# Kernel tuning notes

Measured on AMD Instinct MI355X. Metric: run time of the kernel, lower is better.

Reference implementation:

```python
import jax, jax.numpy as jnp
import numpy as np

K = 9  # 3x3 kernel field

def _conv(x, w, b, pad):
    out = jax.lax.conv_general_dilated(x, w, (1, 1), ((pad, pad), (pad, pad)),
                                       dimension_numbers=('NCHW', 'OIHW', 'NCHW'))
    return out + b[None, :, None, None]

def _conv_transpose(x, w, b):
    # torch ConvTranspose2d(k=3, stride=2, padding=1, output_padding=1); w: [Cin, Cout, 3, 3]
    wk = jnp.flip(jnp.transpose(w, (1, 0, 2, 3)), axis=(2, 3))  # [Cout, Cin, 3, 3]
    out = jax.lax.conv_general_dilated(x, wk, (1, 1), ((1, 2), (1, 2)),
                                       lhs_dilation=(2, 2),
                                       dimension_numbers=('NCHW', 'OIHW', 'NCHW'))
    return out + b[None, :, None, None]

def _modulated_deform_conv(x, offset, mask, w, b):
    # x: [B,C,H,W], offset: [B,2K,H,W] (y,x interleaved per kernel point, row-major),
    # mask: [B,K,H,W], w: [O,C,3,3]; stride=1, pad=1, dilation=1
    B, C, H, W = x.shape
    O = w.shape[0]
    off = offset.reshape(B, K, 2, H, W)
    ky, kx = jnp.meshgrid(jnp.arange(3), jnp.arange(3), indexing='ij')
    base_y = (jnp.arange(H)[None, :, None] - 1 + ky.reshape(K, 1, 1)).astype(x.dtype)  # [K,H,1]
    base_x = (jnp.arange(W)[None, None, :] - 1 + kx.reshape(K, 1, 1)).astype(x.dtype)  # [K,1,W]
    py = off[:, :, 0] + base_y[None]  # [B,K,H,W]
    px = off[:, :, 1] + base_x[None]
    y0 = jnp.floor(py); x0 = jnp.floor(px)
    wy = py - y0; wx = px - x0
    y0i = y0.astype(jnp.int32); x0i = x0.astype(jnp.int32)
    flat = x.reshape(B, C, H * W)

    def gather(yi, xi):
        valid = ((yi >= 0) & (yi < H) & (xi >= 0) & (xi < W)).astype(x.dtype)
        idx = jnp.clip(yi, 0, H - 1) * W + jnp.clip(xi, 0, W - 1)  # [B,K,H,W]
        g = jax.vmap(lambda im, ix: im[:, ix])(flat, idx.reshape(B, -1))  # [B,C,K*H*W]
        return g.reshape(B, C, K, H, W) * valid[:, None]

    v = (gather(y0i, x0i)         * ((1 - wy) * (1 - wx))[:, None]
       + gather(y0i, x0i + 1)     * ((1 - wy) * wx)[:, None]
       + gather(y0i + 1, x0i)     * (wy * (1 - wx))[:, None]
       + gather(y0i + 1, x0i + 1) * (wy * wx)[:, None])
    v = v * mask[:, None]  # modulation
    out = jnp.einsum('bckhw,ock->bohw', v, w.reshape(O, C, K))
    return out + b[None, :, None, None]

def setup_inputs() -> dict:
    key = jax.random.key(0)
    ks = jax.random.split(key, 8)
    B, Cin, Cout, H, W = 4, 128, 64, 64, 64
    return {
        'high_feature': jax.random.normal(ks[0], (B, Cin, H, W), jnp.float32),
        'low_feature': jax.random.normal(ks[1], (B, Cout, 2 * H, 2 * W), jnp.float32),
        'w_up': jax.random.normal(ks[2], (Cin, Cout, 3, 3), jnp.float32) * 0.03,
        'b_up': jnp.zeros((Cout,), jnp.float32),
        'w_off': jax.random.normal(ks[3], (3 * K, 2 * Cout, 3, 3), jnp.float32) * 0.02,
        'b_off': jnp.zeros((3 * K,), jnp.float32),
        'w_align': jax.random.normal(ks[4], (Cout, Cout, 3, 3), jnp.float32) * 0.04,
        'b_align': jnp.zeros((Cout,), jnp.float32),
    }

def reference(high_feature, low_feature, w_up, b_up, w_off, b_off, w_align, b_align):
    up = _conv_transpose(high_feature, w_up, b_up)            # [B,Cout,2H,2W]
    fo = _conv(jnp.concatenate([up, low_feature], axis=1), w_off, b_off, 1)
    offset, mask = fo[:, :2 * K], fo[:, 2 * K:]
    mask = 2.0 * jax.nn.sigmoid(mask)
    aligned = _modulated_deform_conv(up, offset, mask, w_align, b_align)
    aligned = jnp.where(aligned >= 0, aligned, 0.2 * aligned)  # LeakyReLU(0.2)
    return jnp.concatenate([aligned, low_feature], axis=1)
```

## Files before the change

### kernel.cpp

```cpp
#include <hip/hip_runtime.h>
#include <math.h>

namespace {
constexpr int B   = 4;
constexpr int CIN = 128;
constexpr int CO  = 64;
constexpr int HF  = 64;
constexpr int HO  = 128;
constexpr int HW  = HO * HO;
constexpr int NOFF = 27;

constexpr size_t UPB  = 0;
constexpr size_t LOB  = UPB + (size_t)B * HW * CO / 2;
constexpr size_t HBF  = LOB + (size_t)B * HW * CO / 2;
constexpr size_t WFRG = HBF + (size_t)B * HF * HF * CIN / 2;
constexpr size_t WFUP = WFRG + (size_t)(4 * 18 * 64 * 8) / 2;
constexpr size_t WFOF = WFUP + (size_t)(9 * 4 * 4 * 64 * 8) / 2;
}

using half8 = __attribute__((ext_vector_type(8))) _Float16;
using h2    = __attribute__((ext_vector_type(2))) _Float16;
using f32x4 = __attribute__((ext_vector_type(4))) float;

__device__ __forceinline__ unsigned short f2h16(float f) {
  return __builtin_bit_cast(unsigned short, (_Float16)f);
}
__device__ __forceinline__ unsigned pkh(float a, float b) {
  return __builtin_bit_cast(unsigned, __builtin_amdgcn_cvt_pkrtz(a, b));
}
__device__ __forceinline__ h2 u2h(unsigned u) { return __builtin_bit_cast(h2, u); }
__device__ __forceinline__ unsigned h2u(h2 v) { return __builtin_bit_cast(unsigned, v); }
__device__ __forceinline__ h2 dup_lo(unsigned u) {
  return u2h(__builtin_amdgcn_perm(u, u, 0x01000100u));
}
__device__ __forceinline__ h2 dup_hi(unsigned u) {
  return u2h(__builtin_amdgcn_perm(u, u, 0x03020302u));
}

__global__ __launch_bounds__(256) void k_prep(const float* __restrict__ high,
                                              const float* __restrict__ wup,
                                              const float* __restrict__ woff,
                                              const float* __restrict__ wal,
                                              float* __restrict__ ws) {
  __shared__ unsigned short tl2[32][66];
  const int bid = blockIdx.x;
  const int t = threadIdx.x;

  if (bid < 288) {
    int i = bid * 256 + t;
    if (i < 4 * 18 * 64 * 8) {
      int j = i & 7; int t2 = i >> 3;
      int lane = t2 & 63; int t3 = t2 >> 6;
      int kb = t3 % 18; int w = t3 / 18;
      int tap = kb >> 1;
      int c = (kb & 1) * 32 + ((lane >> 4) << 3) + j;
      int o = (w << 4) + (lane & 15);
      unsigned short* wfrag = (unsigned short*)(ws + WFRG);
      wfrag[i] = f2h16(wal[((size_t)o * CO + c) * 9 + tap]);
    }
    if (i < 9 * 4 * 4 * 64 * 8) {
      int j = i & 7; int lane = (i >> 3) & 63; int w = (i >> 9) & 3;
      int ch = (i >> 11) & 3; int rr = i >> 13;
      int c = ch * 32 + ((lane >> 4) << 3) + j;
      int o = w * 16 + (lane & 15);
      unsigned short* wfup = (unsigned short*)(ws + WFUP);
      wfup[i] = f2h16(wup[((size_t)c * CO + o) * 9 + rr]);
    }
    if (i < 9 * 4 * 2 * 64 * 8) {
      int j = i & 7; int lane = (i >> 3) & 63; int nt = (i >> 9) & 1;
      int kc = (i >> 10) & 3; int tap = i >> 12;
      int c = kc * 32 + ((lane >> 4) << 3) + j;
      int o = nt * 16 + (lane & 15);
      float v = 0.f;
      if (o < NOFF) v = woff[(((size_t)o * 2 * CO + c) * 3 + tap / 3) * 3 + (tap % 3)];
      unsigned short* wfo = (unsigned short*)(ws + WFOF);
      wfo[i] = f2h16(v);
    }
    return;
  }

  {
    unsigned short* hbf = (unsigned short*)(ws + HBF);
    int j = bid - 288;
    const int c0 = (j & 3) * 32;
    const int y = (j >> 2) & 63, b = j >> 8;
    const int x = t & 63, clb = t >> 6;
#pragma unroll
    for (int k = 0; k < 8; ++k) {
      int cl = clb * 8 + k;
      float v = high[(((size_t)b * CIN + c0 + cl) * HF + y) * HF + x];
      tl2[cl][x] = f2h16(v);
    }
    __syncthreads();
    int px = t >> 2, cg = t & 3;
    ushort4 a, bb;
    a.x = tl2[cg * 8 + 0][px]; a.y = tl2[cg * 8 + 1][px];
    a.z = tl2[cg * 8 + 2][px]; a.w = tl2[cg * 8 + 3][px];
    bb.x = tl2[cg * 8 + 4][px]; bb.y = tl2[cg * 8 + 5][px];
    bb.z = tl2[cg * 8 + 6][px]; bb.w = tl2[cg * 8 + 7][px];
    unsigned short* dst = hbf + (((size_t)b * HF + y) * HF + px) * CIN + c0 + cg * 8;
    *(ushort4*)(dst) = a;
    *(ushort4*)(dst + 4) = bb;
  }
}

union SmemUp {
  unsigned short At[2][4][85][8];
  float accs[4][16][65];
  unsigned short tl[64][130];
};

__global__ __launch_bounds__(256) void k_up(const float* __restrict__ low,
                                            const float* __restrict__ bup,
                                            float* __restrict__ out,
                                            float* __restrict__ ws) {
  __shared__ SmemUp sm;
  const int t = threadIdx.x;

  if (blockIdx.x >= 1024) {
    unsigned short* lob = (unsigned short*)(ws + LOB);
    int j = blockIdx.x - 1024;
    const int y = j & 127, b = j >> 7;
#pragma unroll
    for (int it = 0; it < 8; ++it) {
      int i = it * 256 + t;
      int c = i >> 5, xi = (i & 31) * 4;
      float4 v = *(const float4*)(low + (((size_t)b * CO + c) * HO + y) * HO + xi);
      *(float4*)(out + (((size_t)b * 2 * CO + CO + c) * HO + y) * HO + xi) = v;
      sm.tl[c][xi + 0] = f2h16(v.x); sm.tl[c][xi + 1] = f2h16(v.y);
      sm.tl[c][xi + 2] = f2h16(v.z); sm.tl[c][xi + 3] = f2h16(v.w);
    }
    __syncthreads();
#pragma unroll
    for (int it = 0; it < 4; ++it) {
      int i = it * 256 + t;
      int x = i >> 3, cg = i & 7;
      unsigned rw[4];
#pragma unroll
      for (int p = 0; p < 4; ++p)
        rw[p] = (unsigned)sm.tl[cg * 8 + 2 * p][x] | ((unsigned)sm.tl[cg * 8 + 2 * p + 1][x] << 16);
      *(uint4*)(lob + (((size_t)b * HO + y) * HO + x) * CO + cg * 8) =
          make_uint4(rw[0], rw[1], rw[2], rw[3]);
    }
    return;
  }

  const unsigned short* hbf = (const unsigned short*)(ws + HBF);
  const uint4* wfu = (const uint4*)(ws + WFUP);
  unsigned short* upb = (unsigned short*)(ws + UPB);

  const int lane = t & 63;
  const int oq   = __builtin_amdgcn_readfirstlane(t >> 6);
  const int orig = blockIdx.x;
  const int tile = ((orig & 7) << 7) + (orig >> 3);
  const int par  = tile & 3;
  const int pyv  = (par >> 1) & 1, pxv = par & 1;
  const int tx   = ((tile >> 2) & 3) * 16;
  const int ty   = ((tile >> 4) & 15) * 4;
  const int b    = tile >> 8;
  const int nty  = pyv + 1, ntx = pxv + 1;

  uint4 s0, s1;
  const int pxA = t >> 2, cgA = t & 3;
  const int i2 = t + 256, pxB = i2 >> 2, cgB = i2 & 3;

  auto load_chunk = [&](int c0) {
    {
      int gy = ty + pxA / 17, gx = tx + pxA % 17;
      s0 = make_uint4(0, 0, 0, 0);
      if (gy < HF && gx < HF)
        s0 = *(const uint4*)(hbf + (((size_t)b * HF + gy) * HF + gx) * CIN + c0 + cgA * 8);
    }
    s1 = make_uint4(0, 0, 0, 0);
    if (pxB < 85) {
      int gy = ty + pxB / 17, gx = tx + pxB % 17;
      if (gy < HF && gx < HF)
        s1 = *(const uint4*)(hbf + (((size_t)b * HF + gy) * HF + gx) * CIN + c0 + cgB * 8);
    }
  };
  auto write_chunk = [&](int buf) {
    *(uint4*)&sm.At[buf][cgA][pxA][0] = s0;
    if (pxB < 85) *(uint4*)&sm.At[buf][cgB][pxB][0] = s1;
  };

  f32x4 acc[4];
#pragma unroll
  for (int mt = 0; mt < 4; ++mt) acc[mt] = {0.f, 0.f, 0.f, 0.f};

  load_chunk(0);
  write_chunk(0);
  __syncthreads();

  union Cvt { uint4 u; half8 h; };
  int buf = 0;
#pragma unroll 1
  for (int ch = 0; ch < 4; ++ch) {
    if (ch < 3) load_chunk((ch + 1) * 32);
#pragma unroll
    for (int ti = 0; ti < 2; ++ti) {
      if (ti < nty) {
#pragma unroll
        for (int tj = 0; tj < 2; ++tj) {
          if (tj < ntx) {
            int ryA = pyv ? 2 - 2 * ti : 1;
            int rxA = pxv ? 2 - 2 * tj : 1;
            int rr = ryA * 3 + rxA;
            Cvt bw; bw.u = wfu[(((size_t)rr * 4 + ch) * 4 + oq) * 64 + lane];
#pragma unroll
            for (int mt = 0; mt < 4; ++mt) {
              Cvt av;
              av.u = *(const uint4*)&sm.At[buf][lane >> 4][(mt + ti) * 17 + (lane & 15) + tj][0];
              acc[mt] = __builtin_amdgcn_mfma_f32_16x16x32_f16(av.h, bw.h, acc[mt], 0, 0, 0);
            }
          }
        }
      }
    }
    if (ch < 3) write_chunk(buf ^ 1);
    __syncthreads();
    buf ^= 1;
  }

#pragma unroll
  for (int mt = 0; mt < 4; ++mt)
#pragma unroll
    for (int r = 0; r < 4; ++r)
      sm.accs[oq][lane & 15][mt * 16 + (lane >> 4) * 4 + r] = acc[mt][r];
  __syncthreads();

  const int yo = 2 * (ty + (lane >> 4)) + pyv;
  const int xo = 2 * (tx + (lane & 15)) + pxv;
  unsigned short* dst = upb + (((size_t)b * HO + yo) * HO + xo) * CO + oq * 16;
  unsigned rw[8];
#pragma unroll
  for (int p = 0; p < 8; ++p) {
    float v0 = sm.accs[oq][2 * p][lane] + bup[oq * 16 + 2 * p];
    float v1 = sm.accs[oq][2 * p + 1][lane] + bup[oq * 16 + 2 * p + 1];
    rw[p] = pkh(v0, v1);
  }
  *(uint4*)dst = make_uint4(rw[0], rw[1], rw[2], rw[3]);
  *(uint4*)(dst + 8) = make_uint4(rw[4], rw[5], rw[6], rw[7]);
}

__global__ __launch_bounds__(256) void k_offdcn(const float* __restrict__ boff,
                                                const float* __restrict__ bal,
                                                float* __restrict__ out,
                                                const float* __restrict__ ws) {
  __shared__ float smem[7936];
  unsigned short* us_in = (unsigned short*)smem;
  float* fo_raw = smem;
  unsigned* prm = (unsigned*)(smem + 2112);
  unsigned short* us_vt = (unsigned short*)(smem + 3840);

  const unsigned short* upb = (const unsigned short*)(ws + UPB);
  const unsigned short* lob = (const unsigned short*)(ws + LOB);
  const uint4* wfo = (const uint4*)(ws + WFOF);
  const uint4* wf  = (const uint4*)(ws + WFRG);

  const int t = threadIdx.x;
  const int lane = t & 63;
  const int w = __builtin_amdgcn_readfirstlane(t >> 6);
  const int mh = w >> 1, nt = w & 1;
  const int oq = w;
  const int orig = blockIdx.x;
  const int tile = ((orig & 7) << 7) + (orig >> 3);
  const int tX = (tile & 7) * 16;
  const int tY = ((tile >> 3) & 31) * 4;
  const int b  = tile >> 8;
  const unsigned short* upB = upb + (size_t)b * HW * CO;

  union Cvt { uint4 u; half8 h; };

  for (int i = t; i < 16 * 108; i += 256) {
    int px = i >> 4, cg = i & 15;
    int gy = tY - 1 + px / 18, gx = tX - 1 + px % 18;
    uint4 v = make_uint4(0, 0, 0, 0);
    if (gy >= 0 && gy < HO && gx >= 0 && gx < HO) {
      const unsigned short* src =
          (cg < 8 ? upb : lob) + (((size_t)b * HO + gy) * HO + gx) * CO + (cg & 7) * 8;
      v = *(const uint4*)src;
    }
    *(uint4*)&us_in[((size_t)cg * 108 + px) * 8] = v;
  }
  __syncthreads();

  f32x4 acc2[2];
  acc2[0] = {0.f, 0.f, 0.f, 0.f}; acc2[1] = {0.f, 0.f, 0.f, 0.f};
#pragma unroll 1
  for (int tap = 0; tap < 9; ++tap) {
    int ky = tap / 3, kx = tap % 3;
#pragma unroll
    for (int kc = 0; kc < 4; ++kc) {
      Cvt bw; bw.u = wfo[(((size_t)tap * 4 + kc) * 2 + nt) * 64 + lane];
#pragma unroll
      for (int mt = 0; mt < 2; ++mt) {
        int sy = mh * 2 + mt;
        Cvt av;
        av.u = *(const uint4*)&us_in[(((size_t)(kc * 4 + (lane >> 4))) * 108 +
                                      (sy + ky) * 18 + (lane & 15) + kx) * 8];
        acc2[mt] = __builtin_amdgcn_mfma_f32_16x16x32_f16(av.h, bw.h, acc2[mt], 0, 0, 0);
      }
    }
  }
  __syncthreads();

#pragma unroll
  for (int mt = 0; mt < 2; ++mt)
#pragma unroll
    for (int r = 0; r < 4; ++r)
      fo_raw[(nt * 16 + (lane & 15)) * 66 + mh * 32 + mt * 16 + (lane >> 4) * 4 + r] =
          acc2[mt][r];
  __syncthreads();

  for (int i = t; i < 9 * 64; i += 256) {
    int k = i >> 6, px = i & 63;
    int y = tY + (px >> 4), x = tX + (px & 15);
    float offy = fo_raw[(2 * k) * 66 + px] + boff[2 * k];
    float offx = fo_raw[(2 * k + 1) * 66 + px] + boff[2 * k + 1];
    float m = 2.f / (1.f + expf(-(fo_raw[(18 + k) * 66 + px] + boff[18 + k])));
    float pyf = offy + (float)(y - 1 + k / 3);
    float pxf = offx + (float)(x - 1 + k % 3);
    float y0f = floorf(pyf), x0f = floorf(pxf);
    float wy = pyf - y0f, wx = pxf - x0f;
    int y0 = (int)y0f, x0 = (int)x0f;
    int y1 = y0 + 1, x1 = x0 + 1;
    float vy0 = (y0 >= 0 && y0 < HO) ? m : 0.f;
    float vy1 = (y1 >= 0 && y1 < HO) ? m : 0.f;
    float vx0 = (x0 >= 0 && x0 < HO) ? 1.f : 0.f;
    float vx1 = (x1 >= 0 && x1 < HO) ? 1.f : 0.f;
    float w0 = (1.f - wy) * (1.f - wx) * vy0 * vx0;
    float w1 = (1.f - wy) * wx * vy0 * vx1;
    float w2 = wy * (1.f - wx) * vy1 * vx0;
    float w3 = wy * wx * vy1 * vx1;
    int cy0 = min(max(y0, 0), HO - 1), cy1 = min(max(y1, 0), HO - 1);
    int cx0 = min(max(x0, 0), HO - 1), cx1 = min(max(x1, 0), HO - 1);
    unsigned pc = (unsigned)cy0 | ((unsigned)cy1 << 8) |
                  ((unsigned)cx0 << 16) | ((unsigned)cx1 << 24);
    unsigned* pr = prm + ((size_t)k * 64 + px) * 3;
    pr[0] = pkh(w0, w1);
    pr[1] = pkh(w2, w3);
    pr[2] = pc;
  }
  __syncthreads();

  uint4 u00[2], u01[2], u10[2], u11[2];

  auto issue = [&](int k) {
#pragma unroll
    for (int it = 0; it < 2; ++it) {
      int j = it * 256 + t;
      int q = j & 7, px = j >> 3;
      unsigned pc = prm[((size_t)k * 64 + px) * 3 + 2];
      int cy0 = pc & 255, cy1 = (pc >> 8) & 255, cx0 = (pc >> 16) & 255, cx1 = pc >> 24;
      const unsigned short* base = upB + q * 8;
      u00[it] = *(const uint4*)(base + (size_t)(cy0 * HO + cx0) * CO);
      u01[it] = *(const uint4*)(base + (size_t)(cy0 * HO + cx1) * CO);
      u10[it] = *(const uint4*)(base + (size_t)(cy1 * HO + cx0) * CO);
      u11[it] = *(const uint4*)(base + (size_t)(cy1 * HO + cx1) * CO);
    }
  };

  auto combine = [&](int k, int buf) {
#pragma unroll
    for (int it = 0; it < 2; ++it) {
      int j = it * 256 + t;
      int q = j & 7, px = j >> 3;
      const unsigned* pr = prm + ((size_t)k * 64 + px) * 3;
      unsigned pw01 = pr[0], pw23 = pr[1];
      h2 w0 = dup_lo(pw01), w1 = dup_hi(pw01);
      h2 w2 = dup_lo(pw23), w3 = dup_hi(pw23);
      unsigned a0[4] = {u00[it].x, u00[it].y, u00[it].z, u00[it].w};
      unsigned a1[4] = {u01[it].x, u01[it].y, u01[it].z, u01[it].w};
      unsigned a2[4] = {u10[it].x, u10[it].y, u10[it].z, u10[it].w};
      unsigned a3[4] = {u11[it].x, u11[it].y, u11[it].z, u11[it].w};
      unsigned rw[4];
#pragma unroll
      for (int p = 0; p < 4; ++p) {
        h2 r = w3 * u2h(a3[p]);
        r = __builtin_elementwise_fma(w2, u2h(a2[p]), r);
        r = __builtin_elementwise_fma(w1, u2h(a1[p]), r);
        r = __builtin_elementwise_fma(w0, u2h(a0[p]), r);
        rw[p] = h2u(r);
      }
      *(uint4*)&us_vt[(((size_t)buf * 8 + q) * 64 + px) * 8] = make_uint4(rw[0], rw[1], rw[2], rw[3]);
    }
  };

  f32x4 acc[4];
#pragma unroll
  for (int mt = 0; mt < 4; ++mt) acc[mt] = {0.f, 0.f, 0.f, 0.f};

  uint4 bw0 = wf[(oq * 18 + 0) * 64 + lane];
  uint4 bw1 = wf[(oq * 18 + 1) * 64 + lane];
  uint4 bn0, bn1;

  issue(0);
  combine(0, 0);
  issue(1);
  __syncthreads();

  int buf = 0;
#pragma unroll 1
  for (int k = 0; k < 9; ++k) {
#pragma unroll
    for (int kb2 = 0; kb2 < 2; ++kb2) {
      Cvt bfr; bfr.u = kb2 ? bw1 : bw0;
#pragma unroll
      for (int mt = 0; mt < 4; ++mt) {
        Cvt av;
        av.u = *(const uint4*)&us_vt[(((size_t)buf * 8 + kb2 * 4 + (lane >> 4)) * 64 +
                                      mt * 16 + (lane & 15)) * 8];
        acc[mt] = __builtin_amdgcn_mfma_f32_16x16x32_f16(av.h, bfr.h, acc[mt], 0, 0, 0);
      }
    }
    if (k < 8) {
      combine(k + 1, buf ^ 1);
      if (k < 7) issue(k + 2);
      bn0 = wf[(oq * 18 + 2 * k + 2) * 64 + lane];
      bn1 = wf[(oq * 18 + 2 * k + 3) * 64 + lane];
    }
    __syncthreads();
    bw0 = bn0; bw1 = bn1;
    buf ^= 1;
  }

  float* accs = smem;
#pragma unroll
  for (int mt = 0; mt < 4; ++mt)
#pragma unroll
    for (int r = 0; r < 4; ++r)
      accs[((size_t)oq * 16 + (lane & 15)) * 65 + mt * 16 + (lane >> 4) * 4 + r] = acc[mt][r];
  __syncthreads();

  const int y = tY + (lane >> 4), x = tX + (lane & 15);
  float* ob = out + (size_t)b * 2 * CO * HW + (size_t)y * HO + x;
#pragma unroll
  for (int ol = 0; ol < 16; ++ol) {
    int o = oq * 16 + ol;
    float v = accs[((size_t)oq * 16 + ol) * 65 + lane] + bal[o];
    v = (v >= 0.f) ? v : 0.2f * v;
    ob[(size_t)o * HW] = v;
  }
}

extern "C" void kernel_launch(void* const* d_in, const int* in_sizes, int n_in,
                              void* d_out, int out_size, void* d_ws, size_t ws_size,
                              hipStream_t stream) {
  const float* high = (const float*)d_in[0];
  const float* low  = (const float*)d_in[1];
  const float* wup  = (const float*)d_in[2];
  const float* bup  = (const float*)d_in[3];
  const float* woff = (const float*)d_in[4];
  const float* boff = (const float*)d_in[5];
  const float* wal  = (const float*)d_in[6];
  const float* bal  = (const float*)d_in[7];
  float* out = (float*)d_out;
  float* ws  = (float*)d_ws;

  k_prep<<<dim3(1312), dim3(256), 0, stream>>>(high, wup, woff, wal, ws);
  k_up<<<dim3(1536), dim3(256), 0, stream>>>(low, bup, out, ws);
  k_offdcn<<<dim3(1024), dim3(256), 0, stream>>>(boff, bal, out, ws);
}
```

Before: 57.73 us.

## Process two deform-conv taps per barrier with deeper gather prefetch

Restructures the deformable-conv main loop so each iteration handles two kernel taps (two LDS slots per buffer) instead of one, with two register sets of bilinear-corner gathers in flight. This halves the number of __syncthreads and keeps more global gathers outstanding so their latency overlaps with MFMA work. In exchange it raises LDS use (12032 floats) and register pressure, which may cut occupancy, and it needs a separate tail step for the ninth tap.

After: 65.96 us. 14.3% more time.

```diff
diff --git a/kernel.cpp b/kernel.cpp
--- a/kernel.cpp
+++ b/kernel.cpp
@@ -246,7 +246,7 @@
                                                 const float* __restrict__ bal,
                                                 float* __restrict__ out,
                                                 const float* __restrict__ ws) {
-  __shared__ float smem[7936];
+  __shared__ float smem[12032];
   unsigned short* us_in = (unsigned short*)smem;
   float* fo_raw = smem;
   unsigned* prm = (unsigned*)(smem + 2112);
@@ -343,9 +343,11 @@
   }
   __syncthreads();
 
-  uint4 u00[2], u01[2], u10[2], u11[2];
-
-  auto issue = [&](int k) {
+  uint4 a00[2], a01[2], a10[2], a11[2];
+  uint4 b00[2], b01[2], b10[2], b11[2];
+
+  auto issue_g = [&](int k, uint4 (&c00)[2], uint4 (&c01)[2],
+                     uint4 (&c10)[2], uint4 (&c11)[2]) {
 #pragma unroll
     for (int it = 0; it < 2; ++it) {
       int j = it * 256 + t;
@@ -353,14 +355,15 @@
       unsigned pc = prm[((size_t)k * 64 + px) * 3 + 2];
       int cy0 = pc & 255, cy1 = (pc >> 8) & 255, cx0 = (pc >> 16) & 255, cx1 = pc >> 24;
       const unsigned short* base = upB + q * 8;
-      u00[it] = *(const uint4*)(base + (size_t)(cy0 * HO + cx0) * CO);
-      u01[it] = *(const uint4*)(base + (size_t)(cy0 * HO + cx1) * CO);
-      u10[it] = *(const uint4*)(base + (size_t)(cy1 * HO + cx0) * CO);
-      u11[it] = *(const uint4*)(base + (size_t)(cy1 * HO + cx1) * CO);
+      c00[it] = *(const uint4*)(base + (size_t)(cy0 * HO + cx0) * CO);
+      c01[it] = *(const uint4*)(base + (size_t)(cy0 * HO + cx1) * CO);
+      c10[it] = *(const uint4*)(base + (size_t)(cy1 * HO + cx0) * CO);
+      c11[it] = *(const uint4*)(base + (size_t)(cy1 * HO + cx1) * CO);
     }
   };
 
-  auto combine = [&](int k, int buf) {
+  auto combine_g = [&](int k, int slot, uint4 (&c00)[2], uint4 (&c01)[2],
+                       uint4 (&c10)[2], uint4 (&c11)[2]) {
 #pragma unroll
     for (int it = 0; it < 2; ++it) {
       int j = it * 256 + t;
@@ -369,20 +372,21 @@
       unsigned pw01 = pr[0], pw23 = pr[1];
       h2 w0 = dup_lo(pw01), w1 = dup_hi(pw01);
       h2 w2 = dup_lo(pw23), w3 = dup_hi(pw23);
-      unsigned a0[4] = {u00[it].x, u00[it].y, u00[it].z, u00[it].w};
-      unsigned a1[4] = {u01[it].x, u01[it].y, u01[it].z, u01[it].w};
-      unsigned a2[4] = {u10[it].x, u10[it].y, u10[it].z, u10[it].w};
-      unsigned a3[4] = {u11[it].x, u11[it].y, u11[it].z, u11[it].w};
+      unsigned q0[4] = {c00[it].x, c00[it].y, c00[it].z, c00[it].w};
+      unsigned q1[4] = {c01[it].x, c01[it].y, c01[it].z, c01[it].w};
+      unsigned q2[4] = {c10[it].x, c10[it].y, c10[it].z, c10[it].w};
+      unsigned q3[4] = {c11[it].x, c11[it].y, c11[it].z, c11[it].w};
       unsigned rw[4];
 #pragma unroll
       for (int p = 0; p < 4; ++p) {
-        h2 r = w3 * u2h(a3[p]);
-        r = __builtin_elementwise_fma(w2, u2h(a2[p]), r);
-        r = __builtin_elementwise_fma(w1, u2h(a1[p]), r);
-        r = __builtin_elementwise_fma(w0, u2h(a0[p]), r);
+        h2 r = w3 * u2h(q3[p]);
+        r = __builtin_elementwise_fma(w2, u2h(q2[p]), r);
+        r = __builtin_elementwise_fma(w1, u2h(q1[p]), r);
+        r = __builtin_elementwise_fma(w0, u2h(q0[p]), r);
         rw[p] = h2u(r);
       }
-      *(uint4*)&us_vt[(((size_t)buf * 8 + q) * 64 + px) * 8] = make_uint4(rw[0], rw[1], rw[2], rw[3]);
+      *(uint4*)&us_vt[(((size_t)slot * 8 + q) * 64 + px) * 8] =
+          make_uint4(rw[0], rw[1], rw[2], rw[3]);
     }
   };
 
@@ -390,39 +394,66 @@
 #pragma unroll
   for (int mt = 0; mt < 4; ++mt) acc[mt] = {0.f, 0.f, 0.f, 0.f};
 
-  uint4 bw0 = wf[(oq * 18 + 0) * 64 + lane];
-  uint4 bw1 = wf[(oq * 18 + 1) * 64 + lane];
-  uint4 bn0, bn1;
-
-  issue(0);
-  combine(0, 0);
-  issue(1);
+  uint4 bw[4], bn[4];
+#pragma unroll
+  for (int q = 0; q < 4; ++q) bw[q] = wf[(oq * 18 + q) * 64 + lane];
+
+  issue_g(0, a00, a01, a10, a11);
+  combine_g(0, 0, a00, a01, a10, a11);
+  issue_g(1, a00, a01, a10, a11);
+  combine_g(1, 1, a00, a01, a10, a11);
+  issue_g(2, a00, a01, a10, a11);
+  issue_g(3, b00, b01, b10, b11);
   __syncthreads();
 
   int buf = 0;
 #pragma unroll 1
-  for (int k = 0; k < 9; ++k) {
-#pragma unroll
-    for (int kb2 = 0; kb2 < 2; ++kb2) {
-      Cvt bfr; bfr.u = kb2 ? bw1 : bw0;
-#pragma unroll
-      for (int mt = 0; mt < 4; ++mt) {
-        Cvt av;
-        av.u = *(const uint4*)&us_vt[(((size_t)buf * 8 + kb2 * 4 + (lane >> 4)) * 64 +
-                                      mt * 16 + (lane & 15)) * 8];
-        acc[mt] = __builtin_amdgcn_mfma_f32_16x16x32_f16(av.h, bfr.h, acc[mt], 0, 0, 0);
+  for (int p = 0; p < 4; ++p) {
+#pragma unroll
+    for (int tp = 0; tp < 2; ++tp) {
+#pragma unroll
+      for (int kb2 = 0; kb2 < 2; ++kb2) {
+        Cvt bfr; bfr.u = bw[tp * 2 + kb2];
+#pragma unroll
+        for (int mt = 0; mt < 4; ++mt) {
+          Cvt av;
+          av.u = *(const uint4*)&us_vt[((((size_t)(buf * 2 + tp)) * 8 + kb2 * 4 +
+                                         (lane >> 4)) * 64 + mt * 16 + (lane & 15)) * 8];
+          acc[mt] = __builtin_amdgcn_mfma_f32_16x16x32_f16(av.h, bfr.h, acc[mt], 0, 0, 0);
+        }
       }
     }
-    if (k < 8) {
-      combine(k + 1, buf ^ 1);
-      if (k < 7) issue(k + 2);
-      bn0 = wf[(oq * 18 + 2 * k + 2) * 64 + lane];
-      bn1 = wf[(oq * 18 + 2 * k + 3) * 64 + lane];
+    if (p < 3) {
+      combine_g(2 * p + 2, (buf ^ 1) * 2 + 0, a00, a01, a10, a11);
+      issue_g(2 * p + 4, a00, a01, a10, a11);
+      combine_g(2 * p + 3, (buf ^ 1) * 2 + 1, b00, b01, b10, b11);
+      if (p < 2) issue_g(2 * p + 5, b00, b01, b10, b11);
+#pragma unroll
+      for (int q = 0; q < 4; ++q) bn[q] = wf[(oq * 18 + (2 * p + 2) * 2 + q) * 64 + lane];
+    } else {
+      combine_g(8, (buf ^ 1) * 2 + 0, a00, a01, a10, a11);
+      bn[0] = wf[(oq * 18 + 16) * 64 + lane];
+      bn[1] = wf[(oq * 18 + 17) * 64 + lane];
+      bn[2] = bn[0]; bn[3] = bn[1];
     }
     __syncthreads();
-    bw0 = bn0; bw1 = bn1;
+#pragma unroll
+    for (int q = 0; q < 4; ++q) bw[q] = bn[q];
     buf ^= 1;
   }
+
+#pragma unroll
+  for (int kb2 = 0; kb2 < 2; ++kb2) {
+    Cvt bfr; bfr.u = bw[kb2];
+#pragma unroll
+    for (int mt = 0; mt < 4; ++mt) {
+      Cvt av;
+      av.u = *(const uint4*)&us_vt[((((size_t)(buf * 2)) * 8 + kb2 * 4 +
+                                     (lane >> 4)) * 64 + mt * 16 + (lane & 15)) * 8];
+      acc[mt] = __builtin_amdgcn_mfma_f32_16x16x32_f16(av.h, bfr.h, acc[mt], 0, 0, 0);
+    }
+  }
+  __syncthreads();
 
   float* accs = smem;
 #pragma unroll
```

## Fuse bilinear gather directly into MFMA A-operand registers, drop LDS staging

Applied to the files above, without the earlier changes.

Each wave now gathers the four bilinear corner vectors for its own MFMA A-fragment, blends them in registers and feeds them straight into the MFMA, removing the shared-memory staging buffer and the per-tap barriers. The goal is to cut LDS traffic, synchronisation and shared memory use, which may raise occupancy. In exchange, all four waves redundantly gather and blend the same sampled values (4x duplicated global loads and FMA work), and the software prefetch that overlapped loads of the next tap with the current MFMAs is gone.

New measurement: 158.6 us. +174.8%, slower.

```diff
diff --git a/kernel.cpp b/kernel.cpp
--- a/kernel.cpp
+++ b/kernel.cpp
@@ -246,11 +246,10 @@
                                                 const float* __restrict__ bal,
                                                 float* __restrict__ out,
                                                 const float* __restrict__ ws) {
-  __shared__ float smem[7936];
+  __shared__ float smem[6912];
   unsigned short* us_in = (unsigned short*)smem;
   float* fo_raw = smem;
   unsigned* prm = (unsigned*)(smem + 2112);
-  unsigned short* us_vt = (unsigned short*)(smem + 3840);
 
   const unsigned short* upb = (const unsigned short*)(ws + UPB);
   const unsigned short* lob = (const unsigned short*)(ws + LOB);
@@ -343,86 +342,55 @@
   }
   __syncthreads();
 
-  uint4 u00[2], u01[2], u10[2], u11[2];
-
-  auto issue = [&](int k) {
-#pragma unroll
-    for (int it = 0; it < 2; ++it) {
-      int j = it * 256 + t;
-      int q = j & 7, px = j >> 3;
-      unsigned pc = prm[((size_t)k * 64 + px) * 3 + 2];
-      int cy0 = pc & 255, cy1 = (pc >> 8) & 255, cx0 = (pc >> 16) & 255, cx1 = pc >> 24;
-      const unsigned short* base = upB + q * 8;
-      u00[it] = *(const uint4*)(base + (size_t)(cy0 * HO + cx0) * CO);
-      u01[it] = *(const uint4*)(base + (size_t)(cy0 * HO + cx1) * CO);
-      u10[it] = *(const uint4*)(base + (size_t)(cy1 * HO + cx0) * CO);
-      u11[it] = *(const uint4*)(base + (size_t)(cy1 * HO + cx1) * CO);
-    }
-  };
-
-  auto combine = [&](int k, int buf) {
-#pragma unroll
-    for (int it = 0; it < 2; ++it) {
-      int j = it * 256 + t;
-      int q = j & 7, px = j >> 3;
-      const unsigned* pr = prm + ((size_t)k * 64 + px) * 3;
-      unsigned pw01 = pr[0], pw23 = pr[1];
+  f32x4 acc[4];
+#pragma unroll
+  for (int mt = 0; mt < 4; ++mt) acc[mt] = {0.f, 0.f, 0.f, 0.f};
+
+  const int qo = (lane >> 4) * 8;
+
+#pragma unroll 1
+  for (int tap = 0; tap < 9; ++tap) {
+    uint4 bq0 = wf[(oq * 18 + 2 * tap) * 64 + lane];
+    uint4 bq1 = wf[(oq * 18 + 2 * tap + 1) * 64 + lane];
+#pragma unroll
+    for (int mt = 0; mt < 4; ++mt) {
+      const int px = mt * 16 + (lane & 15);
+      const unsigned* pr = prm + ((size_t)tap * 64 + px) * 3;
+      unsigned pw01 = pr[0], pw23 = pr[1], pc = pr[2];
       h2 w0 = dup_lo(pw01), w1 = dup_hi(pw01);
       h2 w2 = dup_lo(pw23), w3 = dup_hi(pw23);
-      unsigned a0[4] = {u00[it].x, u00[it].y, u00[it].z, u00[it].w};
-      unsigned a1[4] = {u01[it].x, u01[it].y, u01[it].z, u01[it].w};
-      unsigned a2[4] = {u10[it].x, u10[it].y, u10[it].z, u10[it].w};
-      unsigned a3[4] = {u11[it].x, u11[it].y, u11[it].z, u11[it].w};
-      unsigned rw[4];
-#pragma unroll
-      for (int p = 0; p < 4; ++p) {
-        h2 r = w3 * u2h(a3[p]);
-        r = __builtin_elementwise_fma(w2, u2h(a2[p]), r);
-        r = __builtin_elementwise_fma(w1, u2h(a1[p]), r);
-        r = __builtin_elementwise_fma(w0, u2h(a0[p]), r);
-        rw[p] = h2u(r);
-      }
-      *(uint4*)&us_vt[(((size_t)buf * 8 + q) * 64 + px) * 8] = make_uint4(rw[0], rw[1], rw[2], rw[3]);
-    }
-  };
-
-  f32x4 acc[4];
-#pragma unroll
-  for (int mt = 0; mt < 4; ++mt) acc[mt] = {0.f, 0.f, 0.f, 0.f};
-
-  uint4 bw0 = wf[(oq * 18 + 0) * 64 + lane];
-  uint4 bw1 = wf[(oq * 18 + 1) * 64 + lane];
-  uint4 bn0, bn1;
-
-  issue(0);
-  combine(0, 0);
-  issue(1);
-  __syncthreads();
-
-  int buf = 0;
-#pragma unroll 1
-  for (int k = 0; k < 9; ++k) {
-#pragma unroll
-    for (int kb2 = 0; kb2 < 2; ++kb2) {
-      Cvt bfr; bfr.u = kb2 ? bw1 : bw0;
-#pragma unroll
-      for (int mt = 0; mt < 4; ++mt) {
-        Cvt av;
-        av.u = *(const uint4*)&us_vt[(((size_t)buf * 8 + kb2 * 4 + (lane >> 4)) * 64 +
-                                      mt * 16 + (lane & 15)) * 8];
+      int cy0 = pc & 255, cy1 = (pc >> 8) & 255, cx0 = (pc >> 16) & 255, cx1 = pc >> 24;
+      const unsigned short* p00 = upB + (size_t)(cy0 * HO + cx0) * CO;
+      const unsigned short* p01 = upB + (size_t)(cy0 * HO + cx1) * CO;
+      const unsigned short* p10 = upB + (size_t)(cy1 * HO + cx0) * CO;
+      const unsigned short* p11 = upB + (size_t)(cy1 * HO + cx1) * CO;
+#pragma unroll
+      for (int kb2 = 0; kb2 < 2; ++kb2) {
+        const int o8 = qo + kb2 * 32;
+        uint4 v00 = *(const uint4*)(p00 + o8);
+        uint4 v01 = *(const uint4*)(p01 + o8);
+        uint4 v10 = *(const uint4*)(p10 + o8);
+        uint4 v11 = *(const uint4*)(p11 + o8);
+        unsigned q0[4] = {v00.x, v00.y, v00.z, v00.w};
+        unsigned q1[4] = {v01.x, v01.y, v01.z, v01.w};
+        unsigned q2[4] = {v10.x, v10.y, v10.z, v10.w};
+        unsigned q3[4] = {v11.x, v11.y, v11.z, v11.w};
+        unsigned rw[4];
+#pragma unroll
+        for (int p = 0; p < 4; ++p) {
+          h2 r = w3 * u2h(q3[p]);
+          r = __builtin_elementwise_fma(w2, u2h(q2[p]), r);
+          r = __builtin_elementwise_fma(w1, u2h(q1[p]), r);
+          r = __builtin_elementwise_fma(w0, u2h(q0[p]), r);
+          rw[p] = h2u(r);
+        }
+        Cvt av; av.u = make_uint4(rw[0], rw[1], rw[2], rw[3]);
+        Cvt bfr; bfr.u = kb2 ? bq1 : bq0;
         acc[mt] = __builtin_amdgcn_mfma_f32_16x16x32_f16(av.h, bfr.h, acc[mt], 0, 0, 0);
       }
     }
-    if (k < 8) {
-      combine(k + 1, buf ^ 1);
-      if (k < 7) issue(k + 2);
-      bn0 = wf[(oq * 18 + 2 * k + 2) * 64 + lane];
-      bn1 = wf[(oq * 18 + 2 * k + 3) * 64 + lane];
-    }
-    __syncthreads();
-    bw0 = bn0; bw1 = bn1;
-    buf ^= 1;
-  }
+  }
+  __syncthreads();
 
   float* accs = smem;
 #pragma unroll
```
